# Kernel tuning notes

Hardware: AMD Instinct MI355X
Metric: run time of the kernel (lower is better)

## Reference

```python
import jax, jax.numpy as jnp
import numpy as np

ALPHA = 3.0      # sharpness in tanh(alpha * lin(x)) (HypergraphConstructor)
TOPK = 10        # scale_hyperedges: neighbors per node in similarity topk
NEG_SLOPE = 0.2  # LeakyReLU slope in HypergraphAttention


def setup_inputs() -> dict:
    key = jax.random.key(0)
    ks = jax.random.split(key, 8)
    B, L, N, F, D, E = 16, 64, 512, 64, 64, 40
    return {
        "x": jax.random.normal(ks[0], (B, L, N, F), jnp.float32),
        "idx": jnp.arange(N, dtype=jnp.int64) if jax.config.jax_enable_x64 else jnp.arange(N, dtype=jnp.int32),
        "emb1": 0.1 * jax.random.normal(ks[1], (N, E), jnp.float32),
        "lin1_w": jax.random.normal(ks[2], (E, E), jnp.float32) / np.float32(np.sqrt(E)),
        "lin1_b": jnp.zeros((E,), jnp.float32),
        "W_self": 0.1 * jax.random.normal(ks[3], (F, D), jnp.float32),
        "W_neigh": 0.1 * jax.random.normal(ks[4], (F, D), jnp.float32),
        "W_concat": 0.1 * jax.random.normal(ks[5], (2 * D, D), jnp.float32),
        "attention": 0.1 * jax.random.normal(ks[6], (2 * D, 1), jnp.float32),
    }


def build_incidence(idx, emb1, lin1_w, lin1_b):
    """HypergraphConstructor (similarity-topk branch). Returns H: (N_nodes, M_hyperedges)."""
    feats = jnp.tanh(ALPHA * (emb1[idx] @ lin1_w + lin1_b))        # (N, E)
    sim = feats @ feats.T                                          # (N, N)
    _, top = jax.lax.top_k(sim, TOPK)                              # (N, k) indices
    n = feats.shape[0]
    rows = jnp.arange(n)[:, None]
    H = jnp.zeros((n, n), feats.dtype).at[rows, top].set(1.0)      # row i = hyperedge from node i's neighbors
    return H.T                                                     # (N nodes, M hyperedges)


def hypergraph_attention(x, H, W_self, W_neigh, W_concat, attention):
    """Faithful HypergraphAttention.forward (eval mode: dropout is identity)."""
    x_self = jnp.einsum('blnf,fd->blnd', x, W_self)
    # aggregate nodes -> hyperedges: H.T[m,n] == H[n,m]
    he = jnp.einsum('nm,blnf->blmf', H, x)                          # (B, L, M, F)
    e_deg = jnp.maximum(H.sum(axis=0), 1.0)                        # (M,)
    he = he / e_deg[None, None, :, None]
    he = jnp.where(he >= 0, he, NEG_SLOPE * he)                    # LeakyReLU(0.2)
    # scatter hyperedges -> nodes
    x_neigh = jnp.einsum('nm,blmf->blnf', H, he)                   # (B, L, N, F)
    n_deg = jnp.maximum(H.sum(axis=1), 1.0)                        # (N,)
    x_neigh = x_neigh / n_deg[None, None, :, None]
    x_neigh = jnp.einsum('blnf,fd->blnd', x_neigh, W_neigh)
    x_cat = jnp.concatenate([x_self, x_neigh], axis=-1)            # (B, L, N, 2D)
    scores = jnp.squeeze(x_cat @ attention, axis=-1)               # (B, L, N)
    w = jax.nn.softmax(scores, axis=-1)                            # softmax over nodes
    return (x_cat * w[..., None]) @ W_concat                       # (B, L, N, D)


def reference(x, idx, emb1, lin1_w, lin1_b, W_self, W_neigh, W_concat, attention):
    H = build_incidence(idx, emb1, lin1_w, lin1_b)
    return hypergraph_attention(x, H, W_self, W_neigh, W_concat, attention)
```

## Files before the change

### kernel.cpp

```cpp
#include <hip/hip_runtime.h>

#define N_NODES 512
#define E_DIM   40
#define TOPK    10

typedef unsigned short u16;
typedef __attribute__((ext_vector_type(8))) short short8;
typedef __attribute__((ext_vector_type(4))) float f32x4;

__device__ __forceinline__ u16 f2bf(float f) {
    unsigned int b = __float_as_uint(f);
    b += 0x7fffu + ((b >> 16) & 1u);
    return (u16)(b >> 16);
}
__device__ __forceinline__ float bf2f(u16 u) {
    return __uint_as_float(((unsigned int)u) << 16);
}
__device__ __forceinline__ unsigned pk2(float a, float b) {
    return (unsigned)f2bf(a) | ((unsigned)f2bf(b) << 16);
}

__global__ void prep_kernel(const float* __restrict__ emb1,
                            const float* __restrict__ w,
                            const float* __restrict__ b,
                            float* __restrict__ feats,
                            const float* __restrict__ Ws, const float* __restrict__ Wn,
                            const float* __restrict__ Wc, const float* __restrict__ att,
                            u16* __restrict__ Wt, float* __restrict__ ap) {
    if (blockIdx.x < N_NODES) {
        int n = blockIdx.x, e = threadIdx.x;
        if (e >= E_DIM) return;
        const float* er = emb1 + n * E_DIM;
        float s = b[e];
        for (int k = 0; k < E_DIM; ++k) s += er[k] * w[k * E_DIM + e];
        feats[n * E_DIM + e] = tanhf(3.0f * s);
    } else {
        int f = blockIdx.x - N_NODES, d = threadIdx.x;
        float a = 0.f, bb = 0.f;
        for (int k = 0; k < 64; ++k) {
            a  += Ws[f * 64 + k] * Wc[k * 64 + d];
            bb += Wn[f * 64 + k] * Wc[(64 + k) * 64 + d];
        }
        Wt[d * 128 + f]      = f2bf(a);
        Wt[d * 128 + 64 + f] = f2bf(bb);
        float p0 = Ws[f * 64 + d] * att[d];
        float p1 = Wn[f * 64 + d] * att[64 + d];
        for (int off = 32; off > 0; off >>= 1) {
            p0 += __shfl_down(p0, off);
            p1 += __shfl_down(p1, off);
        }
        if (d == 0) { ap[f] = p0; ap[64 + f] = p1; }
    }
}

#define TOPK_SMEM (512 * 41 * 4 + 4 * 512 * 4)

__global__ __launch_bounds__(256) void topk_kernel(const float* __restrict__ feats,
                                                   u16* __restrict__ top16) {
    extern __shared__ float tsm[];
    float* sf   = tsm;
    float* ssim = tsm + 512 * 41;
    const int tid = threadIdx.x;
    for (int i = tid; i < 512 * E_DIM; i += 256) {
        int n = i / E_DIM, k = i - n * E_DIM;
        sf[n * 41 + k] = feats[i];
    }
    __syncthreads();
    const int wv = tid >> 6, lane = tid & 63;
    const int m = blockIdx.x * 4 + wv;
    float* sim = ssim + wv * 512;

    float fm[E_DIM];
#pragma unroll
    for (int k = 0; k < E_DIM; ++k) fm[k] = sf[m * 41 + k];
    for (int n = lane; n < N_NODES; n += 64) {
        const float* fr = &sf[n * 41];
        float s = 0.f;
#pragma unroll
        for (int k = 0; k < E_DIM; ++k) s += fm[k] * fr[k];
        sim[n] = s;
    }
    __syncthreads();
    for (int it = 0; it < TOPK; ++it) {
        float bv = -3.0e38f; int bi = 1 << 30;
        for (int n = lane; n < N_NODES; n += 64) {
            float v = sim[n];
            if (v > bv) { bv = v; bi = n; }
        }
        for (int off = 32; off > 0; off >>= 1) {
            float ov = __shfl_down(bv, off);
            int   oi = __shfl_down(bi, off);
            if (ov > bv || (ov == bv && oi < bi)) { bv = ov; bi = oi; }
        }
        bi = __shfl(bi, 0);
        if (lane == 0) top16[m * 16 + it] = (u16)bi;
        __syncthreads();
        sim[bi] = -3.0e38f;
        __syncthreads();
    }
}

__global__ void hbuild_kernel(const u16* __restrict__ top16,
                              u16* __restrict__ Hrow, u16* __restrict__ H,
                              int* __restrict__ deg) {
    int m = threadIdx.x;
#pragma unroll
    for (int j = 0; j < TOPK; ++j) {
        int n = (int)top16[m * 16 + j];
        Hrow[m * 512 + n] = 0x3F80;
        H[n * 512 + m]    = 0x3F80;
        atomicAdd(&deg[n], 1);
    }
}

#define SC_OFF  65536
#define RED_OFF 67584
#define SMEM_BYTES 67648

__device__ __forceinline__ int rm_byte(int n, int g) {
    return n * 128 + ((g ^ (n & 7)) << 4);
}
__device__ __forceinline__ int t64_byte(int f, int g) {
    return f * 1024 + ((g ^ (f & 7)) << 4);
}

__global__ __launch_bounds__(512, 4) void main_kernel(
    const float* __restrict__ x,
    const u16* __restrict__ Hrow, const u16* __restrict__ H,
    const int* __restrict__ deg,
    const u16* __restrict__ Wt, const float* __restrict__ ap,
    float* __restrict__ out)
{
    extern __shared__ char smem[];
    float* sc  = (float*)(smem + SC_OFF);
    float* red = (float*)(smem + RED_OFF);

    const int bl  = blockIdx.x;
    const int tid = threadIdx.x;
    const int wv = tid >> 6, lane = tid & 63;
    const int lrow = lane & 15, lk = lane >> 4;
    const float* xr   = x   + (size_t)bl * N_NODES * 64;
    float*       outr = out + (size_t)bl * N_NODES * 64;

    float s = 0.f;
    {
        const float4* px = (const float4*)(xr + tid * 64);
        const int gcol = tid >> 3, bcol = (tid & 7) * 2;
#pragma unroll
        for (int g = 0; g < 8; ++g) {
            float4 v0 = px[2 * g], v1 = px[2 * g + 1];
            float4 a0 = *(const float4*)(ap + g * 8);
            float4 a1 = *(const float4*)(ap + g * 8 + 4);
            s += v0.x * a0.x + v0.y * a0.y + v0.z * a0.z + v0.w * a0.w
               + v1.x * a1.x + v1.y * a1.y + v1.z * a1.z + v1.w * a1.w;
            float vf[8] = { v0.x, v0.y, v0.z, v0.w, v1.x, v1.y, v1.z, v1.w };
#pragma unroll
            for (int j = 0; j < 8; ++j) {
                int f = g * 8 + j;
                *(u16*)(smem + t64_byte(f, gcol) + bcol) = f2bf(vf[j]);
            }
        }
    }
    __syncthreads();

    {
        f32x4 acc[4][4];
#pragma unroll
        for (int mt = 0; mt < 4; ++mt)
#pragma unroll
            for (int ft = 0; ft < 4; ++ft) acc[mt][ft] = (f32x4)0.f;
        for (int ks = 0; ks < 16; ++ks) {
            short8 afr[4], bfr[4];
#pragma unroll
            for (int mt = 0; mt < 4; ++mt)
                afr[mt] = *(const short8*)(Hrow + (wv * 64 + mt * 16 + lrow) * 512
                                                + ks * 32 + lk * 8);
#pragma unroll
            for (int ft = 0; ft < 4; ++ft)
                bfr[ft] = *(const short8*)(smem + t64_byte(ft * 16 + lrow, ks * 4 + lk));
#pragma unroll
            for (int mt = 0; mt < 4; ++mt)
#pragma unroll
                for (int ft = 0; ft < 4; ++ft)
                    acc[mt][ft] = __builtin_amdgcn_mfma_f32_16x16x32_bf16(
                        afr[mt], bfr[ft], acc[mt][ft], 0, 0, 0);
        }
        __syncthreads();
#pragma unroll
        for (int mt = 0; mt < 4; ++mt) {
            const int gm = wv * 8 + mt * 2 + (lk >> 1);
#pragma unroll
            for (int ft = 0; ft < 4; ++ft) {
                const int f = ft * 16 + lrow;
                float v[4];
#pragma unroll
                for (int r = 0; r < 4; ++r) {
                    float t = acc[mt][ft][r] * 0.1f;
                    v[r] = t >= 0.f ? t : 0.2f * t;
                }
                *(uint2*)(smem + t64_byte(f, gm) + (lk & 1) * 8) =
                    make_uint2(pk2(v[0], v[1]), pk2(v[2], v[3]));
            }
        }
    }
    __syncthreads();

    {
        f32x4 acc[4][4];
#pragma unroll
        for (int nt = 0; nt < 4; ++nt)
#pragma unroll
            for (int ft = 0; ft < 4; ++ft) acc[nt][ft] = (f32x4)0.f;
        for (int ks = 0; ks < 16; ++ks) {
            short8 afr[4], bfr[4];
#pragma unroll
            for (int ft = 0; ft < 4; ++ft)
                afr[ft] = *(const short8*)(smem + t64_byte(ft * 16 + lrow, ks * 4 + lk));
#pragma unroll
            for (int nt = 0; nt < 4; ++nt)
                bfr[nt] = *(const short8*)(H + (wv * 64 + nt * 16 + lrow) * 512
                                             + ks * 32 + lk * 8);
#pragma unroll
            for (int nt = 0; nt < 4; ++nt)
#pragma unroll
                for (int ft = 0; ft < 4; ++ft)
                    acc[nt][ft] = __builtin_amdgcn_mfma_f32_16x16x32_bf16(
                        afr[ft], bfr[nt], acc[nt][ft], 0, 0, 0);
        }
        __syncthreads();
#pragma unroll
        for (int nt = 0; nt < 4; ++nt) {
            const int n = wv * 64 + nt * 16 + lrow;
            int dg = deg[n];
            const float ideg = 1.0f / (float)(dg > 0 ? dg : 1);
#pragma unroll
            for (int ft = 0; ft < 4; ++ft) {
                const int gf = ft * 2 + (lk >> 1);
                *(uint2*)(smem + rm_byte(n, gf) + (lk & 1) * 8) =
                    make_uint2(pk2(acc[nt][ft][0] * ideg, acc[nt][ft][1] * ideg),
                               pk2(acc[nt][ft][2] * ideg, acc[nt][ft][3] * ideg));
            }
        }
    }
    __syncthreads();

#pragma unroll
    for (int g = 0; g < 8; ++g) {
        short8 q = *(const short8*)(smem + rm_byte(tid, g));
        float4 b0 = *(const float4*)(ap + 64 + g * 8);
        float4 b1 = *(const float4*)(ap + 64 + g * 8 + 4);
        s += bf2f((u16)q[0]) * b0.x + bf2f((u16)q[1]) * b0.y
           + bf2f((u16)q[2]) * b0.z + bf2f((u16)q[3]) * b0.w
           + bf2f((u16)q[4]) * b1.x + bf2f((u16)q[5]) * b1.y
           + bf2f((u16)q[6]) * b1.z + bf2f((u16)q[7]) * b1.w;
    }
    float bv = s;
#pragma unroll
    for (int off = 32; off > 0; off >>= 1) bv = fmaxf(bv, __shfl_xor(bv, off));
    if (lane == 0) red[wv] = bv;
    __syncthreads();
    float M = red[0];
#pragma unroll
    for (int w = 1; w < 8; ++w) M = fmaxf(M, red[w]);
    float ev = expf(s - M);
    sc[tid] = ev;
    float sv = ev;
#pragma unroll
    for (int off = 32; off > 0; off >>= 1) sv += __shfl_xor(sv, off);
    if (lane == 0) red[8 + wv] = sv;
    __syncthreads();
    float S = red[8];
#pragma unroll
    for (int w = 1; w < 8; ++w) S += red[8 + w];
    const float invS = 1.0f / S;

    {
        for (int nt = 0; nt < 4; ++nt) {
            const int n = wv * 64 + nt * 16 + lrow;
            f32x4 accn[4];
#pragma unroll
            for (int dt = 0; dt < 4; ++dt) accn[dt] = (f32x4)0.f;
#pragma unroll
            for (int ks = 0; ks < 4; ++ks) {
                short8 bfrag;
                if (ks < 2) {
                    const float4* px = (const float4*)(xr + n * 64 + ks * 32 + lk * 8);
                    float4 v0 = px[0], v1 = px[1];
                    union { uint4 u; short8 s8; } cv;
                    cv.u.x = pk2(v0.x, v0.y); cv.u.y = pk2(v0.z, v0.w);
                    cv.u.z = pk2(v1.x, v1.y); cv.u.w = pk2(v1.z, v1.w);
                    bfrag = cv.s8;
                } else {
                    int gx = (ks - 2) * 4 + lk;
                    bfrag = *(const short8*)(smem + rm_byte(n, gx));
                }
#pragma unroll
                for (int dt = 0; dt < 4; ++dt) {
                    short8 wfrag = *(const short8*)(Wt + (dt * 16 + lrow) * 128
                                                       + ks * 32 + lk * 8);
                    accn[dt] = __builtin_amdgcn_mfma_f32_16x16x32_bf16(
                        wfrag, bfrag, accn[dt], 0, 0, 0);
                }
            }
            const float ww = sc[n] * invS;
#pragma unroll
            for (int dt = 0; dt < 4; ++dt) {
                float4 f;
                f.x = accn[dt][0] * ww; f.y = accn[dt][1] * ww;
                f.z = accn[dt][2] * ww; f.w = accn[dt][3] * ww;
                *(float4*)(outr + n * 64 + dt * 16 + lk * 4) = f;
            }
        }
    }
}

#define WS_FEATS 0
#define WS_TOP   81920
#define WS_WT    98304
#define WS_AP    114688
#define WS_DEG   115200
#define WS_HROW  131072
#define WS_H     655360
#define WS_END   1179648

extern "C" void kernel_launch(void* const* d_in, const int* in_sizes, int n_in,
                              void* d_out, int out_size, void* d_ws, size_t ws_size,
                              hipStream_t stream) {
    const float* x        = (const float*)d_in[0];
    const float* emb1     = (const float*)d_in[2];
    const float* lin1_w   = (const float*)d_in[3];
    const float* lin1_b   = (const float*)d_in[4];
    const float* W_self   = (const float*)d_in[5];
    const float* W_neigh  = (const float*)d_in[6];
    const float* W_concat = (const float*)d_in[7];
    const float* att      = (const float*)d_in[8];
    float* out = (float*)d_out;

    char* ws = (char*)d_ws;
    float* feats = (float*)(ws + WS_FEATS);
    u16*   top16 = (u16*)  (ws + WS_TOP);
    u16*   Wt    = (u16*)  (ws + WS_WT);
    float* ap    = (float*)(ws + WS_AP);
    int*   deg   = (int*)  (ws + WS_DEG);
    u16*   Hrow  = (u16*)  (ws + WS_HROW);
    u16*   H     = (u16*)  (ws + WS_H);

    prep_kernel<<<N_NODES + 64, 64, 0, stream>>>(emb1, lin1_w, lin1_b, feats,
                                                 W_self, W_neigh, W_concat, att, Wt, ap);

    (void)hipFuncSetAttribute((const void*)topk_kernel,
                              hipFuncAttributeMaxDynamicSharedMemorySize, TOPK_SMEM);
    topk_kernel<<<128, 256, TOPK_SMEM, stream>>>(feats, top16);

    (void)hipMemsetAsync(ws + WS_DEG, 0, WS_END - WS_DEG, stream);
    hbuild_kernel<<<1, 512, 0, stream>>>(top16, Hrow, H, deg);

    (void)hipFuncSetAttribute((const void*)main_kernel,
                              hipFuncAttributeMaxDynamicSharedMemorySize, SMEM_BYTES);
    main_kernel<<<1024, 512, SMEM_BYTES, stream>>>(x, Hrow, H, deg, Wt, ap, out);
}
```

Measured before the change: 243.7 us.

## Split hyperedge GEMMs into two feature halves with a split-layout x_neigh buffer

```diff
diff --git a/kernel.cpp b/kernel.cpp
--- a/kernel.cpp
+++ b/kernel.cpp
@@ -117,11 +117,11 @@
 #define RED_OFF 67584
 #define SMEM_BYTES 67648
 
-__device__ __forceinline__ int rm_byte(int n, int g) {
-    return n * 128 + ((g ^ (n & 7)) << 4);
-}
 __device__ __forceinline__ int t64_byte(int f, int g) {
     return f * 1024 + ((g ^ (f & 7)) << 4);
+}
+__device__ __forceinline__ int xnr_byte(int n, int g) {
+    return ((g >> 2) << 15) + n * 64 + (((g & 3) ^ (n & 3)) << 4);
 }
 
 __global__ __launch_bounds__(512, 4) void main_kernel(
@@ -163,39 +163,41 @@
     }
     __syncthreads();
 
-    {
-        f32x4 acc[4][4];
+#pragma unroll
+    for (int half = 0; half < 2; ++half) {
+        f32x4 acc[4][2];
 #pragma unroll
         for (int mt = 0; mt < 4; ++mt)
 #pragma unroll
-            for (int ft = 0; ft < 4; ++ft) acc[mt][ft] = (f32x4)0.f;
+            for (int fh = 0; fh < 2; ++fh) acc[mt][fh] = (f32x4)0.f;
         for (int ks = 0; ks < 16; ++ks) {
-            short8 afr[4], bfr[4];
+            short8 afr[4], bfr[2];
 #pragma unroll
             for (int mt = 0; mt < 4; ++mt)
                 afr[mt] = *(const short8*)(Hrow + (wv * 64 + mt * 16 + lrow) * 512
                                                 + ks * 32 + lk * 8);
 #pragma unroll
-            for (int ft = 0; ft < 4; ++ft)
-                bfr[ft] = *(const short8*)(smem + t64_byte(ft * 16 + lrow, ks * 4 + lk));
+            for (int fh = 0; fh < 2; ++fh)
+                bfr[fh] = *(const short8*)(smem +
+                              t64_byte((half * 2 + fh) * 16 + lrow, ks * 4 + lk));
 #pragma unroll
             for (int mt = 0; mt < 4; ++mt)
 #pragma unroll
-                for (int ft = 0; ft < 4; ++ft)
-                    acc[mt][ft] = __builtin_amdgcn_mfma_f32_16x16x32_bf16(
-                        afr[mt], bfr[ft], acc[mt][ft], 0, 0, 0);
+                for (int fh = 0; fh < 2; ++fh)
+                    acc[mt][fh] = __builtin_amdgcn_mfma_f32_16x16x32_bf16(
+                        afr[mt], bfr[fh], acc[mt][fh], 0, 0, 0);
         }
         __syncthreads();
 #pragma unroll
         for (int mt = 0; mt < 4; ++mt) {
             const int gm = wv * 8 + mt * 2 + (lk >> 1);
 #pragma unroll
-            for (int ft = 0; ft < 4; ++ft) {
-                const int f = ft * 16 + lrow;
+            for (int fh = 0; fh < 2; ++fh) {
+                const int f = (half * 2 + fh) * 16 + lrow;
                 float v[4];
 #pragma unroll
                 for (int r = 0; r < 4; ++r) {
-                    float t = acc[mt][ft][r] * 0.1f;
+                    float t = acc[mt][fh][r] * 0.1f;
                     v[r] = t >= 0.f ? t : 0.2f * t;
                 }
                 *(uint2*)(smem + t64_byte(f, gm) + (lk & 1) * 8) =
@@ -205,17 +207,19 @@
     }
     __syncthreads();
 
-    {
-        f32x4 acc[4][4];
+#pragma unroll
+    for (int half = 0; half < 2; ++half) {
+        f32x4 acc[4][2];
 #pragma unroll
         for (int nt = 0; nt < 4; ++nt)
 #pragma unroll
-            for (int ft = 0; ft < 4; ++ft) acc[nt][ft] = (f32x4)0.f;
+            for (int fh = 0; fh < 2; ++fh) acc[nt][fh] = (f32x4)0.f;
         for (int ks = 0; ks < 16; ++ks) {
-            short8 afr[4], bfr[4];
-#pragma unroll
-            for (int ft = 0; ft < 4; ++ft)
-                afr[ft] = *(const short8*)(smem + t64_byte(ft * 16 + lrow, ks * 4 + lk));
+            short8 afr[2], bfr[4];
+#pragma unroll
+            for (int fh = 0; fh < 2; ++fh)
+                afr[fh] = *(const short8*)(smem +
+                              t64_byte((half * 2 + fh) * 16 + lrow, ks * 4 + lk));
 #pragma unroll
             for (int nt = 0; nt < 4; ++nt)
                 bfr[nt] = *(const short8*)(H + (wv * 64 + nt * 16 + lrow) * 512
@@ -223,9 +227,9 @@
 #pragma unroll
             for (int nt = 0; nt < 4; ++nt)
 #pragma unroll
-                for (int ft = 0; ft < 4; ++ft)
-                    acc[nt][ft] = __builtin_amdgcn_mfma_f32_16x16x32_bf16(
-                        afr[ft], bfr[nt], acc[nt][ft], 0, 0, 0);
+                for (int fh = 0; fh < 2; ++fh)
+                    acc[nt][fh] = __builtin_amdgcn_mfma_f32_16x16x32_bf16(
+                        afr[fh], bfr[nt], acc[nt][fh], 0, 0, 0);
         }
         __syncthreads();
 #pragma unroll
@@ -234,11 +238,11 @@
             int dg = deg[n];
             const float ideg = 1.0f / (float)(dg > 0 ? dg : 1);
 #pragma unroll
-            for (int ft = 0; ft < 4; ++ft) {
-                const int gf = ft * 2 + (lk >> 1);
-                *(uint2*)(smem + rm_byte(n, gf) + (lk & 1) * 8) =
-                    make_uint2(pk2(acc[nt][ft][0] * ideg, acc[nt][ft][1] * ideg),
-                               pk2(acc[nt][ft][2] * ideg, acc[nt][ft][3] * ideg));
+            for (int fh = 0; fh < 2; ++fh) {
+                const int g = (half * 2 + fh) * 2 + (lk >> 1);
+                *(uint2*)(smem + xnr_byte(n, g) + (lk & 1) * 8) =
+                    make_uint2(pk2(acc[nt][fh][0] * ideg, acc[nt][fh][1] * ideg),
+                               pk2(acc[nt][fh][2] * ideg, acc[nt][fh][3] * ideg));
             }
         }
     }
@@ -246,7 +250,7 @@
 
 #pragma unroll
     for (int g = 0; g < 8; ++g) {
-        short8 q = *(const short8*)(smem + rm_byte(tid, g));
+        short8 q = *(const short8*)(smem + xnr_byte(tid, g));
         float4 b0 = *(const float4*)(ap + 64 + g * 8);
         float4 b1 = *(const float4*)(ap + 64 + g * 8 + 4);
         s += bf2f((u16)q[0]) * b0.x + bf2f((u16)q[1]) * b0.y
@@ -292,7 +296,7 @@
                     bfrag = cv.s8;
                 } else {
                     int gx = (ks - 2) * 4 + lk;
-                    bfrag = *(const short8*)(smem + rm_byte(n, gx));
+                    bfrag = *(const short8*)(smem + xnr_byte(n, gx));
                 }
 #pragma unroll
                 for (int dt = 0; dt < 4; ++dt) {
```

New measurement: 364.5 us. +49.6%, slower.
